# Kernel optimization log

Measured on AMD Instinct MI355X. Metric: run time of the kernel, lower is better.

## Reference

```python
import jax, jax.numpy as jnp
import numpy as np

N, E, C, NE, G, T = 20000, 320000, 32, 10, 64, 1000
NB, HID, LAYERS = 8, 64, 2
R_MAX, P_CUT, AVG_NEIGH = 5.0, 6, 16.0
LM = 16  # (max_ell+1)^2 spherical-harmonic components
L_OF_LM = jnp.array([0,1,1,1,2,2,2,2,2,3,3,3,3,3,3,3])


def sph_harm(u):
    # component-normalized real spherical harmonics up to l=3 on unit vectors u [E,3]
    x, y, z = u[:, 0], u[:, 1], u[:, 2]
    s3, s15, s5, s105, s7 = 3**0.5, 15**0.5, 5**0.5, 105**0.5, 7**0.5
    s35_8, s21_8 = (35.0/8.0)**0.5, (21.0/8.0)**0.5
    comps = [jnp.ones_like(x),
             s3*x, s3*y, s3*z,
             s15*x*y, s15*y*z, 0.5*s5*(3*z*z-1.0), s15*x*z, 0.5*s15*(x*x-y*y),
             s35_8*y*(3*x*x-y*y), s105*x*y*z, s21_8*y*(5*z*z-1.0),
             0.5*s7*(5*z*z*z-3*z), s21_8*x*(5*z*z-1.0),
             0.5*s105*z*(x*x-y*y), s35_8*x*(x*x-3*y*y)]
    return jnp.stack(comps, axis=-1)  # [E,16]


def radial_embed(r):
    # Bessel basis with polynomial cutoff (MACE RadialEmbeddingBlock)
    n = jnp.arange(1, NB + 1, dtype=r.dtype)
    rc = jnp.maximum(r, 1e-9)
    bessel = (2.0/R_MAX)**0.5 * jnp.sin(n[None, :]*jnp.pi*rc[:, None]/R_MAX) / rc[:, None]
    xr = r / R_MAX
    p = float(P_CUT)
    f = (1.0 - 0.5*(p+1)*(p+2)*xr**p + p*(p+2)*xr**(p+1) - 0.5*p*(p+1)*xr**(p+2))
    f = f * (xr < 1.0)
    return bessel * f[:, None]  # [E,NB]


def setup_inputs():
    key = jax.random.key(0)
    ks = jax.random.split(key, 16)
    positions = jax.random.normal(ks[0], (N, 3)) * 3.0
    species = jax.random.randint(ks[1], (N,), 0, NE)
    node_attrs = jax.nn.one_hot(species, NE, dtype=jnp.float32)
    edge_index = jax.random.randint(ks[2], (2, E), 0, N)
    shifts = jnp.zeros((E, 3), jnp.float32)
    batch = jnp.sort(jax.random.randint(ks[3], (N,), 0, G))
    t = jax.random.randint(ks[4], (G,), 0, T)
    eps = jax.random.normal(ks[5], (N, NE + 3))
    betas = jnp.linspace(1e-4, 0.02, T)
    alpha_bar = jnp.cumprod(1.0 - betas)
    sc = 0.1
    W_embed = sc * jax.random.normal(ks[6], (NE + 1, C))
    W_r1 = sc * jax.random.normal(ks[7], (LAYERS, NB, HID))
    W_r2 = sc * jax.random.normal(ks[8], (LAYERS, HID, C * 4))
    W_mix = sc * jax.random.normal(ks[9], (LAYERS, 4, C, C))
    W_sc = sc * jax.random.normal(ks[10], (NE, C))
    W_prod = sc * jax.random.normal(ks[11], (LAYERS, 3, C))
    W_ro_s = sc * jax.random.normal(ks[12], (LAYERS, C, NE))
    W_ro_v = sc * jax.random.normal(ks[13], (LAYERS, C))
    return {"positions": positions, "node_attrs": node_attrs, "shifts": shifts,
            "eps": eps, "alpha_bar": alpha_bar, "W_embed": W_embed, "W_r1": W_r1,
            "W_r2": W_r2, "W_mix": W_mix, "W_sc": W_sc, "W_prod": W_prod,
            "W_ro_s": W_ro_s, "W_ro_v": W_ro_v, "edge_index": edge_index,
            "batch": batch, "t": t}


def reference(positions, node_attrs, shifts, eps, alpha_bar, W_embed, W_r1, W_r2,
              W_mix, W_sc, W_prod, W_ro_s, W_ro_v, edge_index, batch, t):
    sender, receiver = edge_index[0], edge_index[1]
    # diffusion: noise positions and attrs (DDPM q(x_t|x_0))
    ab = alpha_bar[t][batch][:, None]                       # [N,1]
    attrs0 = node_attrs / 4.0
    pos_noisy = jnp.sqrt(ab) * positions + jnp.sqrt(1.0 - ab) * eps[:, -3:]
    attrs_noisy = jnp.sqrt(ab) * attrs0 + jnp.sqrt(1.0 - ab) * eps[:, :NE]
    tf = (t.astype(jnp.float32) / T)[batch][:, None]
    h = jnp.concatenate([attrs_noisy, tf], axis=-1) @ W_embed  # [N,C]
    # edge geometry
    vec = pos_noisy[receiver] - pos_noisy[sender] + shifts
    r = jnp.sqrt(jnp.sum(vec * vec, axis=-1) + 1e-12)
    Y = sph_harm(vec / r[:, None])                          # [E,16]
    ef = radial_embed(r)                                    # [E,NB]
    scalar = h
    pred = jnp.zeros((N, NE + 3), h.dtype)
    for layer in range(LAYERS):
        rw = jax.nn.silu(ef @ W_r1[layer]) @ W_r2[layer]    # [E,4C]
        rw = rw.reshape(E, C, 4)[:, :, L_OF_LM]             # [E,C,16]
        msg = rw * scalar[sender][:, :, None] * Y[:, None, :]
        agg = jax.ops.segment_sum(msg, receiver, num_segments=N) / AVG_NEIGH
        Wm = W_mix[layer][L_OF_LM]                          # [16,C,C]
        feats = jnp.einsum('nck,kcd->ndk', agg, Wm)         # per-l channel mix
        s = feats[:, :, 0]
        poly = W_prod[layer, 0] + W_prod[layer, 1] * s + W_prod[layer, 2] * s * s
        feats = feats * poly[:, :, None]                    # correlation-3 product
        if layer == 0:
            feats = feats.at[:, :, 0].add(attrs_noisy @ W_sc)  # element skip
        scalar = feats[:, :, 0]
        pred_s = scalar @ W_ro_s[layer]                     # [N,NE]
        pred_v = jnp.einsum('ncm,c->nm', feats[:, :, 1:4], W_ro_v[layer])  # [N,3]
        pred = pred + jnp.concatenate([pred_s, pred_v], axis=-1)
    err = (pred - eps) ** 2
    loss_pos = jax.ops.segment_sum(err[:, -3:].sum(-1), batch, num_segments=G)
    loss_lab = jax.ops.segment_sum(err[:, :NE].sum(-1), batch, num_segments=G)
    nn = jax.ops.segment_sum(jnp.ones((N,), pred.dtype), batch, num_segments=G)
    loss = 0.5 * (loss_pos + loss_lab) / (jnp.maximum(nn, 1.0) * (3 + NE))
    return loss
```

## Files before the change

### kernel.cpp

```cpp
#include <hip/hip_runtime.h>

typedef unsigned short ushort_t;
typedef unsigned int uint_t;

#define NN 20000
#define EE 320000
#define CC 32
#define NEL 10
#define GG 64
#define TTT 1000
#define NBB 8
#define HIDD 64
#define EPB 256
#define NTILE (EE / 16)

typedef __attribute__((ext_vector_type(8))) short bf16x8;
typedef __attribute__((ext_vector_type(4))) float f32x4;

__device__ __forceinline__ float bits2f(uint_t b) { union { uint_t u; float f; } v; v.u = b; return v.f; }
__device__ __forceinline__ ushort_t f2b(float f) {
  union { float f; uint_t u; } v; v.f = f;
  uint_t r = (v.u + 0x7fffu + ((v.u >> 16) & 1u)) >> 16;
  return (ushort_t)r;
}
__device__ __forceinline__ uint_t pk(float a, float b) {
  return (uint_t)f2b(a) | ((uint_t)f2b(b) << 16);
}
__device__ __forceinline__ float lo16(uint_t u) { return bits2f(u << 16); }
__device__ __forceinline__ float hi16(uint_t u) { return bits2f(u & 0xffff0000u); }

__global__ __launch_bounds__(256) void k_prep(
    const float* __restrict__ positions, const float* __restrict__ node_attrs,
    const float* __restrict__ eps, const float* __restrict__ alpha_bar,
    const float* __restrict__ W_embed, const float* __restrict__ W_sc,
    const int* __restrict__ batch, const int* __restrict__ tarr,
    float* __restrict__ pos_noisy, float* __restrict__ scalA,
    float* __restrict__ sc_skip, float* __restrict__ pred, int* __restrict__ deg)
{
  int n = blockIdx.x * 256 + threadIdx.x;
  if (n >= NN) return;
  deg[n] = 0;
  int g = batch[n];
  int tn = tarr[g];
  float ab = alpha_bar[tn];
  float sa = sqrtf(ab), sb = sqrtf(fmaxf(1.0f - ab, 0.0f));
#pragma unroll
  for (int j = 0; j < 3; ++j)
    pos_noisy[n * 3 + j] = sa * positions[n * 3 + j] + sb * eps[n * 13 + 10 + j];
  float an[10];
#pragma unroll
  for (int j = 0; j < 10; ++j)
    an[j] = sa * 0.25f * node_attrs[n * 10 + j] + sb * eps[n * 13 + j];
  float tf = (float)tn * (1.0f / (float)TTT);
  for (int d = 0; d < CC; ++d) {
    float h = tf * W_embed[10 * CC + d];
    float sk = 0.0f;
#pragma unroll
    for (int j = 0; j < 10; ++j) {
      h = fmaf(an[j], W_embed[j * CC + d], h);
      sk = fmaf(an[j], W_sc[j * CC + d], sk);
    }
    scalA[n * CC + d] = h;
    sc_skip[n * CC + d] = sk;
  }
#pragma unroll
  for (int j = 0; j < 13; ++j) pred[n * 13 + j] = 0.0f;
}

__global__ __launch_bounds__(256) void k_edge_deg(const int* __restrict__ ei,
    int* __restrict__ deg)
{
  int e = blockIdx.x * 256 + threadIdx.x;
  atomicAdd(&deg[ei[EE + e]], 1);
}

__global__ __launch_bounds__(1024) void k_scan(const int* __restrict__ deg,
    int* __restrict__ offs, int* __restrict__ cursor,
    float* __restrict__ lnum, float* __restrict__ lcnt)
{
  __shared__ int wsums[16];
  __shared__ int woffs[16];
  int tid = threadIdx.x, lane = tid & 63, wv = tid >> 6;
  if (tid < GG) { lnum[tid] = 0.0f; lcnt[tid] = 0.0f; }
  int base = tid * 20;
  int loc[20];
  int s = 0;
#pragma unroll
  for (int j = 0; j < 20; ++j) {
    int idx = base + j;
    int v = (idx < NN) ? deg[idx] : 0;
    loc[j] = s; s += v;
  }
  int inc = s;
  for (int o = 1; o < 64; o <<= 1) {
    int v = __shfl_up(inc, o, 64);
    if (lane >= o) inc += v;
  }
  if (lane == 63) wsums[wv] = inc;
  __syncthreads();
  if (wv == 0 && lane < 16) {
    int v = wsums[lane];
    int i2 = v;
    for (int o = 1; o < 16; o <<= 1) {
      int vv = __shfl_up(i2, o, 16);
      if (lane >= o) i2 += vv;
    }
    woffs[lane] = i2 - v;
  }
  __syncthreads();
  int texcl = woffs[wv] + (inc - s);
#pragma unroll
  for (int j = 0; j < 20; ++j) {
    int idx = base + j;
    if (idx < NN) { int v = texcl + loc[j]; offs[idx] = v; cursor[idx] = v; }
  }
  if (tid == 1023) offs[NN] = EE;
}

__global__ __launch_bounds__(256) void k_edge2(
    const float* __restrict__ pos_noisy, const float* __restrict__ shifts,
    const int* __restrict__ ei, int* __restrict__ cursor,
    ushort_t* __restrict__ Ys, ushort_t* __restrict__ efs, int* __restrict__ snds)
{
  int e = blockIdx.x * 256 + threadIdx.x;
  int snd = ei[e], rcv = ei[EE + e];
  float vx = pos_noisy[rcv * 3 + 0] - pos_noisy[snd * 3 + 0] + shifts[e * 3 + 0];
  float vy = pos_noisy[rcv * 3 + 1] - pos_noisy[snd * 3 + 1] + shifts[e * 3 + 1];
  float vz = pos_noisy[rcv * 3 + 2] - pos_noisy[snd * 3 + 2] + shifts[e * 3 + 2];
  float r2 = vx * vx + vy * vy + vz * vz + 1e-12f;
  float r = sqrtf(r2);
  float inv = 1.0f / r;
  float x = vx * inv, y = vy * inv, z = vz * inv;

  const float s3 = 1.7320508075688772f, s15 = 3.872983346207417f, s5 = 2.23606797749979f;
  const float s105 = 10.246950765959598f, s7 = 2.6457513110645907f;
  const float s35_8 = 2.091650066335189f, s21_8 = 1.6201851746019651f;
  float yv[16];
  yv[0] = 1.0f;
  yv[1] = s3 * x; yv[2] = s3 * y; yv[3] = s3 * z;
  yv[4] = s15 * x * y;
  yv[5] = s15 * y * z;
  yv[6] = 0.5f * s5 * (3.0f * z * z - 1.0f);
  yv[7] = s15 * x * z;
  yv[8] = 0.5f * s15 * (x * x - y * y);
  yv[9] = s35_8 * y * (3.0f * x * x - y * y);
  yv[10] = s105 * x * y * z;
  yv[11] = s21_8 * y * (5.0f * z * z - 1.0f);
  yv[12] = 0.5f * s7 * (5.0f * z * z * z - 3.0f * z);
  yv[13] = s21_8 * x * (5.0f * z * z - 1.0f);
  yv[14] = 0.5f * s105 * z * (x * x - y * y);
  yv[15] = s35_8 * x * (x * x - 3.0f * y * y);

  float rc = fmaxf(r, 1e-9f);
  float pref = 0.6324555320336759f / rc;
  float th = 0.6283185307179586f * rc;
  float s1 = __sinf(th), c1 = __cosf(th);
  float xr = r * 0.2f;
  float fcut = 0.0f;
  if (xr < 1.0f) {
    float x2 = xr * xr, x3 = x2 * xr;
    float x6 = x3 * x3, x7 = x6 * xr, x8 = x7 * xr;
    fcut = 1.0f - 28.0f * x6 + 48.0f * x7 - 21.0f * x8;
  }
  float efv[8];
  float sp = 0.0f, scur = s1, c2 = 2.0f * c1;
#pragma unroll
  for (int b = 0; b < 8; ++b) {
    efv[b] = pref * scur * fcut;
    float nx = c2 * scur - sp;
    sp = scur; scur = nx;
  }

  int slot = atomicAdd(&cursor[rcv], 1);
  snds[slot] = snd;
  uint4* Y4 = (uint4*)Ys;
  Y4[(size_t)slot * 2 + 0] = make_uint4(pk(yv[0], yv[1]), pk(yv[2], yv[3]),
                                        pk(yv[4], yv[5]), pk(yv[6], yv[7]));
  Y4[(size_t)slot * 2 + 1] = make_uint4(pk(yv[8], yv[9]), pk(yv[10], yv[11]),
                                        pk(yv[12], yv[13]), pk(yv[14], yv[15]));
  ((uint4*)efs)[slot] = make_uint4(pk(efv[0], efv[1]), pk(efv[2], efv[3]),
                                   pk(efv[4], efv[5]), pk(efv[6], efv[7]));
}

__global__ __launch_bounds__(256) void k_ytr(const ushort_t* __restrict__ Ys,
    ushort_t* __restrict__ YT)
{
  int idx = blockIdx.x * 256 + threadIdx.x;
  int tile = idx >> 4, k = idx & 15;
  ushort_t v[16];
#pragma unroll
  for (int el = 0; el < 16; ++el)
    v[el] = Ys[(size_t)(tile * 16 + el) * 16 + k];
  uint_t u[8];
#pragma unroll
  for (int p = 0; p < 8; ++p) u[p] = (uint_t)v[2 * p] | ((uint_t)v[2 * p + 1] << 16);
  uint4* o = (uint4*)(YT + (size_t)tile * 256 + (size_t)k * 16);
  o[0] = make_uint4(u[0], u[1], u[2], u[3]);
  o[1] = make_uint4(u[4], u[5], u[6], u[7]);
}

__global__ __launch_bounds__(256) void k_rw_mfma(
    const ushort_t* __restrict__ efs, const float* __restrict__ W_r1,
    const float* __restrict__ W_r2, const int* __restrict__ snds,
    const float* __restrict__ scal_in, ushort_t* __restrict__ rwT, int layer)
{
  __shared__ __align__(16) ushort_t w2t[128][72];
  __shared__ __align__(16) ushort_t h1[EPB][72];
  int tid = threadIdx.x;
  const float* W1g = W_r1 + layer * NBB * HIDD;
  const float* W2g = W_r2 + layer * HIDD * 128;
  for (int idx = tid; idx < HIDD * 128; idx += 256) {
    int k = idx >> 7, n = idx & 127;
    w2t[n][k] = f2b(W2g[idx]);
  }
  {
    int e = blockIdx.x * EPB + tid;
    uint4 q = ((const uint4*)efs)[e];
    float efr[8] = {lo16(q.x), hi16(q.x), lo16(q.y), hi16(q.y),
                    lo16(q.z), hi16(q.z), lo16(q.w), hi16(q.w)};
    for (int hc = 0; hc < 8; ++hc) {
      float v[8];
#pragma unroll
      for (int hh = 0; hh < 8; ++hh) {
        int h = hc * 8 + hh;
        float t = 0.0f;
#pragma unroll
        for (int b = 0; b < 8; ++b) t = fmaf(efr[b], W1g[b * HIDD + h], t);
        v[hh] = t / (1.0f + __expf(-t));
      }
      *(uint4*)&h1[tid][hc * 8] = make_uint4(pk(v[0], v[1]), pk(v[2], v[3]),
                                             pk(v[4], v[5]), pk(v[6], v[7]));
    }
  }
  __syncthreads();
  int w = tid >> 6, lane = tid & 63;
  int c = lane & 15, quad = lane >> 4;
  bf16x8 bfr[16];
#pragma unroll
  for (int nt = 0; nt < 8; ++nt)
#pragma unroll
    for (int kt = 0; kt < 2; ++kt)
      bfr[nt * 2 + kt] = *(const bf16x8*)&w2t[nt * 16 + c][kt * 32 + quad * 8];
  int mb0 = w * 64;
#pragma unroll
  for (int mt = 0; mt < 4; ++mt) {
    int mbase = mb0 + mt * 16;
    bf16x8 a0 = *(const bf16x8*)&h1[mbase + c][quad * 8];
    bf16x8 a1 = *(const bf16x8*)&h1[mbase + c][32 + quad * 8];
    size_t erow = (size_t)blockIdx.x * EPB + mbase + quad * 4;
    int4 sn = *(const int4*)&snds[erow];
    const float* sb0 = scal_in + (size_t)sn.x * CC;
    const float* sb1 = scal_in + (size_t)sn.y * CC;
    const float* sb2 = scal_in + (size_t)sn.z * CC;
    const float* sb3 = scal_in + (size_t)sn.w * CC;
    int tile = blockIdx.x * 16 + w * 4 + mt;
#pragma unroll
    for (int nt = 0; nt < 8; ++nt) {
      f32x4 acc = {0.0f, 0.0f, 0.0f, 0.0f};
      acc = __builtin_amdgcn_mfma_f32_16x16x32_bf16(a0, bfr[nt * 2 + 0], acc, 0, 0, 0);
      acc = __builtin_amdgcn_mfma_f32_16x16x32_bf16(a1, bfr[nt * 2 + 1], acc, 0, 0, 0);
      int col = nt * 16 + c;
      int cc = col >> 2;
      uint2 st;
      st.x = pk(acc[0] * sb0[cc], acc[1] * sb1[cc]);
      st.y = pk(acc[2] * sb2[cc], acc[3] * sb3[cc]);
      *(uint2*)(rwT + (size_t)tile * 2048 + (size_t)col * 16 + quad * 4) = st;
    }
  }
}

__global__ __launch_bounds__(256) void k_layer(
    const ushort_t* __restrict__ YT, const ushort_t* __restrict__ rwT,
    float* __restrict__ scal_out,
    const int* __restrict__ offs,
    const float* __restrict__ W_mix, const float* __restrict__ W_prod,
    const float* __restrict__ W_ro_s, const float* __restrict__ W_ro_v,
    const float* __restrict__ sc_skip, float* __restrict__ pred, int layer)
{
  __shared__ float lagg[4][CC][16];
  __shared__ float lf[4][CC][4];
  int w = threadIdx.x >> 6, lane = threadIdx.x & 63;
  int n = blockIdx.x * 4 + w;
  int c = lane & 15, quad = lane >> 4;
  int i0 = offs[n], i1 = offs[n + 1];
  int t0 = i0 >> 4, t1 = (i1 + 15) >> 4;
  int tsel = quad >> 1, half8 = quad & 1;
  f32x4 acc[8];
#pragma unroll
  for (int mt = 0; mt < 8; ++mt) acc[mt] = (f32x4){0.0f, 0.0f, 0.0f, 0.0f};

  for (int t = t0; t < t1; t += 2) {
    int ta = t + tsel;
    bf16x8 a[8];
    bf16x8 b;
    bool tv = (ta * 16 < i1) && (ta * 16 + 16 > i0);
    if (tv) {
      const bf16x8* ap = (const bf16x8*)rwT + (size_t)ta * 256 + c * 2 + half8;
#pragma unroll
      for (int mt = 0; mt < 8; ++mt) a[mt] = ap[mt * 32];
      b = ((const bf16x8*)YT)[(size_t)ta * 32 + c * 2 + half8];
      if (ta * 16 < i0 || ta * 16 + 16 > i1) {
        int sbase = ta * 16 + half8 * 8;
#pragma unroll
        for (int j = 0; j < 8; ++j) {
          int s = sbase + j;
          if (s < i0 || s >= i1) b[j] = 0;
        }
      }
    } else {
#pragma unroll
      for (int mt = 0; mt < 8; ++mt) a[mt] = (bf16x8){0, 0, 0, 0, 0, 0, 0, 0};
      b = (bf16x8){0, 0, 0, 0, 0, 0, 0, 0};
    }
#pragma unroll
    for (int mt = 0; mt < 8; ++mt)
      acc[mt] = __builtin_amdgcn_mfma_f32_16x16x32_bf16(a[mt], b, acc[mt], 0, 0, 0);
  }

  int lc = (c >= 1) + (c >= 4) + (c >= 9);
  const float inva = 1.0f / 16.0f;
#pragma unroll
  for (int mt = 0; mt < 8; ++mt) {
    float v = (lc == 0) ? acc[mt][0] : (lc == 1) ? acc[mt][1]
            : (lc == 2) ? acc[mt][2] : acc[mt][3];
    lagg[w][mt * 4 + quad][c] = v * inva;
  }
  __syncthreads();

  int c2 = lane >> 1;
  int kh = lane & 1;
  int kb = kh * 8;
  int d = c2;
  float ft[8] = {0, 0, 0, 0, 0, 0, 0, 0};
  const float* Wm = W_mix + layer * 4096;
  for (int cc2 = 0; cc2 < CC; ++cc2) {
    float m0 = Wm[cc2 * CC + d];
    float m1 = Wm[1024 + cc2 * CC + d];
    float m2 = Wm[2048 + cc2 * CC + d];
    float m3 = Wm[3072 + cc2 * CC + d];
    float u0 = kh ? m2 : m0;
    float u13 = kh ? m3 : m1;
    float u47 = kh ? m3 : m2;
    ft[0] = fmaf(lagg[w][cc2][kb + 0], u0, ft[0]);
    ft[1] = fmaf(lagg[w][cc2][kb + 1], u13, ft[1]);
    ft[2] = fmaf(lagg[w][cc2][kb + 2], u13, ft[2]);
    ft[3] = fmaf(lagg[w][cc2][kb + 3], u13, ft[3]);
    ft[4] = fmaf(lagg[w][cc2][kb + 4], u47, ft[4]);
    ft[5] = fmaf(lagg[w][cc2][kb + 5], u47, ft[5]);
    ft[6] = fmaf(lagg[w][cc2][kb + 6], u47, ft[6]);
    ft[7] = fmaf(lagg[w][cc2][kb + 7], u47, ft[7]);
  }
  float sv = __shfl(ft[0], lane & 62, 64);
  const float* Wp = W_prod + layer * 96;
  float p0 = Wp[d], p1 = Wp[32 + d], p2 = Wp[64 + d];
  float poly = fmaf(fmaf(p2, sv, p1), sv, p0);
#pragma unroll
  for (int j = 0; j < 8; ++j) ft[j] *= poly;
  if (layer == 0 && kh == 0) ft[0] += sc_skip[n * CC + d];
  if (kh == 0) {
    scal_out[n * CC + d] = ft[0];
    lf[w][d][0] = ft[0]; lf[w][d][1] = ft[1]; lf[w][d][2] = ft[2]; lf[w][d][3] = ft[3];
  }
  __syncthreads();
  if (lane < 13) {
    float sum = 0.0f;
    if (lane < 10) {
      const float* Wr = W_ro_s + layer * CC * NEL;
      for (int dd = 0; dd < CC; ++dd) sum = fmaf(lf[w][dd][0], Wr[dd * NEL + lane], sum);
    } else {
      int mm = lane - 10;
      const float* Wv = W_ro_v + layer * CC;
      for (int dd = 0; dd < CC; ++dd) sum = fmaf(lf[w][dd][1 + mm], Wv[dd], sum);
    }
    pred[n * 13 + lane] += sum;
  }
}

__global__ __launch_bounds__(256) void k_loss(const float* __restrict__ pred,
    const float* __restrict__ eps, const int* __restrict__ batch,
    float* __restrict__ lnum, float* __restrict__ lcnt)
{
  __shared__ float psum[GG];
  __shared__ int pcnt[GG];
  int tid = threadIdx.x;
  if (tid < GG) { psum[tid] = 0.0f; pcnt[tid] = 0; }
  __syncthreads();
  int n = blockIdx.x * 256 + tid;
  if (n < NN) {
    int g = batch[n];
    float sum = 0.0f;
#pragma unroll
    for (int j = 0; j < 13; ++j) {
      float dlt = pred[n * 13 + j] - eps[n * 13 + j];
      sum = fmaf(dlt, dlt, sum);
    }
    atomicAdd(&psum[g], sum);
    atomicAdd(&pcnt[g], 1);
  }
  __syncthreads();
  if (tid < GG && pcnt[tid] > 0) {
    atomicAdd(&lnum[tid], psum[tid]);
    atomicAdd(&lcnt[tid], (float)pcnt[tid]);
  }
}

__global__ void k_final(const float* __restrict__ lnum, const float* __restrict__ lcnt,
    float* __restrict__ out)
{
  int g = threadIdx.x;
  if (g < GG) {
    float nn = fmaxf(lcnt[g], 1.0f);
    out[g] = 0.5f * lnum[g] / (nn * 13.0f);
  }
}

extern "C" void kernel_launch(void* const* d_in, const int* in_sizes, int n_in,
                              void* d_out, int out_size, void* d_ws, size_t ws_size,
                              hipStream_t stream) {
  const float* positions  = (const float*)d_in[0];
  const float* node_attrs = (const float*)d_in[1];
  const float* shifts     = (const float*)d_in[2];
  const float* eps        = (const float*)d_in[3];
  const float* alpha_bar  = (const float*)d_in[4];
  const float* W_embed    = (const float*)d_in[5];
  const float* W_r1       = (const float*)d_in[6];
  const float* W_r2       = (const float*)d_in[7];
  const float* W_mix      = (const float*)d_in[8];
  const float* W_sc       = (const float*)d_in[9];
  const float* W_prod     = (const float*)d_in[10];
  const float* W_ro_s     = (const float*)d_in[11];
  const float* W_ro_v     = (const float*)d_in[12];
  const int* edge_index   = (const int*)d_in[13];
  const int* batch        = (const int*)d_in[14];
  const int* tarr         = (const int*)d_in[15];
  float* out = (float*)d_out;

  char* ws = (char*)d_ws;
  size_t off = 0;
  auto alloc = [&](size_t bytes) -> void* {
    void* p = ws + off;
    off = (off + bytes + 255) & ~(size_t)255;
    return p;
  };
  float* pos_noisy = (float*)alloc(NN * 3 * 4);
  float* scalA     = (float*)alloc(NN * CC * 4);
  float* scalB     = (float*)alloc(NN * CC * 4);
  float* sc_skip   = (float*)alloc(NN * CC * 4);
  float* pred      = (float*)alloc(NN * 13 * 4);
  ushort_t* Ys     = (ushort_t*)alloc((size_t)EE * 16 * 2);
  ushort_t* YT     = (ushort_t*)alloc((size_t)NTILE * 256 * 2);
  ushort_t* efs    = (ushort_t*)alloc((size_t)EE * 8 * 2);
  int* snds        = (int*)alloc((size_t)EE * 4);
  ushort_t* rwT    = (ushort_t*)alloc((size_t)NTILE * 2048 * 2);
  int* deg         = (int*)alloc(NN * 4);
  int* offs        = (int*)alloc((NN + 1) * 4);
  int* cursor      = (int*)alloc(NN * 4);
  float* lnum      = (float*)alloc(GG * 4);
  float* lcnt      = (float*)alloc(GG * 4);
  (void)ws_size; (void)in_sizes; (void)n_in; (void)out_size;

  const int NB_N = (NN + 255) / 256;
  const int NB_E = EE / 256;

  k_prep<<<NB_N, 256, 0, stream>>>(positions, node_attrs, eps, alpha_bar, W_embed,
                                   W_sc, batch, tarr, pos_noisy, scalA, sc_skip, pred, deg);
  k_edge_deg<<<NB_E, 256, 0, stream>>>(edge_index, deg);
  k_scan<<<1, 1024, 0, stream>>>(deg, offs, cursor, lnum, lcnt);
  k_edge2<<<NB_E, 256, 0, stream>>>(pos_noisy, shifts, edge_index, cursor, Ys, efs, snds);
  k_ytr<<<NB_E, 256, 0, stream>>>(Ys, YT);

  for (int layer = 0; layer < 2; ++layer) {
    const float* sin_p = (layer == 0) ? scalA : scalB;
    float* sout_p      = (layer == 0) ? scalB : scalA;
    k_rw_mfma<<<NB_E, 256, 0, stream>>>(efs, W_r1, W_r2, snds, sin_p, rwT, layer);
    k_layer<<<NN / 4, 256, 0, stream>>>(YT, rwT, sout_p, offs,
                                        W_mix, W_prod, W_ro_s, W_ro_v,
                                        sc_skip, pred, layer);
  }

  k_loss<<<NB_N, 256, 0, stream>>>(pred, eps, batch, lnum, lcnt);
  k_final<<<1, 64, 0, stream>>>(lnum, lcnt, out);
}
```

Before: 333.1 us.

## Fuse radial MLP into per-node aggregation using padded 16-edge CSR segments

Pads each node's CSR segment to a multiple of 16 edges, so every 16-edge tile belongs to exactly one receiver, and zero-fills the padding slots. The radial MLP and sender-scalar weighting now run inside the per-node aggregation kernel, so the large rwT intermediate is never written to or read back from global memory. W_r2 is pre-packed to bf16 once for both layers. The cost is extra padded work, up to roughly double the edge slots in the worst case, per-wave MFMAs that keep only half the K lanes busy, and load imbalance across nodes of different degree.

```diff
diff --git a/kernel.cpp b/kernel.cpp
--- a/kernel.cpp
+++ b/kernel.cpp
@@ -11,8 +11,7 @@
 #define TTT 1000
 #define NBB 8
 #define HIDD 64
-#define EPB 256
-#define NTILE (EE / 16)
+#define SLOTMAX 620032
 
 typedef __attribute__((ext_vector_type(8))) short bf16x8;
 typedef __attribute__((ext_vector_type(4))) float f32x4;
@@ -67,6 +66,15 @@
   for (int j = 0; j < 13; ++j) pred[n * 13 + j] = 0.0f;
 }
 
+__global__ __launch_bounds__(256) void k_wpack(const float* __restrict__ W_r2,
+    ushort_t* __restrict__ w2tg)
+{
+  int idx = blockIdx.x * 256 + threadIdx.x;
+  int l = idx >> 13, r = idx & 8191;
+  int n = r >> 6, k = r & 63;
+  w2tg[idx] = f2b(W_r2[l * 8192 + k * 128 + n]);
+}
+
 __global__ __launch_bounds__(256) void k_edge_deg(const int* __restrict__ ei,
     int* __restrict__ deg)
 {
@@ -88,7 +96,7 @@
 #pragma unroll
   for (int j = 0; j < 20; ++j) {
     int idx = base + j;
-    int v = (idx < NN) ? deg[idx] : 0;
+    int v = (idx < NN) ? ((deg[idx] + 15) & ~15) : 0;
     loc[j] = s; s += v;
   }
   int inc = s;
@@ -114,7 +122,25 @@
     int idx = base + j;
     if (idx < NN) { int v = texcl + loc[j]; offs[idx] = v; cursor[idx] = v; }
   }
-  if (tid == 1023) offs[NN] = EE;
+  if (tid == 1023) offs[NN] = texcl + s;
+}
+
+__global__ __launch_bounds__(256) void k_pad(const int* __restrict__ deg,
+    const int* __restrict__ offs, ushort_t* __restrict__ Ys,
+    ushort_t* __restrict__ efs, int* __restrict__ snds)
+{
+  int n = blockIdx.x * 256 + threadIdx.x;
+  if (n >= NN) return;
+  int d = deg[n];
+  int pd = (d + 15) & ~15;
+  int s0 = offs[n] + d, s1 = offs[n] + pd;
+  uint4 z = make_uint4(0, 0, 0, 0);
+  for (int s = s0; s < s1; ++s) {
+    ((uint4*)Ys)[(size_t)s * 2 + 0] = z;
+    ((uint4*)Ys)[(size_t)s * 2 + 1] = z;
+    ((uint4*)efs)[s] = z;
+    snds[s] = 0;
+  }
 }
 
 __global__ __launch_bounds__(256) void k_edge2(
@@ -183,10 +209,11 @@
 }
 
 __global__ __launch_bounds__(256) void k_ytr(const ushort_t* __restrict__ Ys,
-    ushort_t* __restrict__ YT)
+    ushort_t* __restrict__ YT, const int* __restrict__ offs)
 {
   int idx = blockIdx.x * 256 + threadIdx.x;
   int tile = idx >> 4, k = idx & 15;
+  if (tile * 16 >= offs[NN]) return;
   ushort_t v[16];
 #pragma unroll
   for (int el = 0; el < 16; ++el)
@@ -199,122 +226,96 @@
   o[1] = make_uint4(u[4], u[5], u[6], u[7]);
 }
 
-__global__ __launch_bounds__(256) void k_rw_mfma(
-    const ushort_t* __restrict__ efs, const float* __restrict__ W_r1,
-    const float* __restrict__ W_r2, const int* __restrict__ snds,
-    const float* __restrict__ scal_in, ushort_t* __restrict__ rwT, int layer)
-{
-  __shared__ __align__(16) ushort_t w2t[128][72];
-  __shared__ __align__(16) ushort_t h1[EPB][72];
-  int tid = threadIdx.x;
-  const float* W1g = W_r1 + layer * NBB * HIDD;
-  const float* W2g = W_r2 + layer * HIDD * 128;
-  for (int idx = tid; idx < HIDD * 128; idx += 256) {
-    int k = idx >> 7, n = idx & 127;
-    w2t[n][k] = f2b(W2g[idx]);
-  }
-  {
-    int e = blockIdx.x * EPB + tid;
-    uint4 q = ((const uint4*)efs)[e];
-    float efr[8] = {lo16(q.x), hi16(q.x), lo16(q.y), hi16(q.y),
-                    lo16(q.z), hi16(q.z), lo16(q.w), hi16(q.w)};
-    for (int hc = 0; hc < 8; ++hc) {
-      float v[8];
-#pragma unroll
-      for (int hh = 0; hh < 8; ++hh) {
-        int h = hc * 8 + hh;
-        float t = 0.0f;
-#pragma unroll
-        for (int b = 0; b < 8; ++b) t = fmaf(efr[b], W1g[b * HIDD + h], t);
-        v[hh] = t / (1.0f + __expf(-t));
-      }
-      *(uint4*)&h1[tid][hc * 8] = make_uint4(pk(v[0], v[1]), pk(v[2], v[3]),
-                                             pk(v[4], v[5]), pk(v[6], v[7]));
-    }
-  }
-  __syncthreads();
-  int w = tid >> 6, lane = tid & 63;
-  int c = lane & 15, quad = lane >> 4;
-  bf16x8 bfr[16];
-#pragma unroll
-  for (int nt = 0; nt < 8; ++nt)
-#pragma unroll
-    for (int kt = 0; kt < 2; ++kt)
-      bfr[nt * 2 + kt] = *(const bf16x8*)&w2t[nt * 16 + c][kt * 32 + quad * 8];
-  int mb0 = w * 64;
-#pragma unroll
-  for (int mt = 0; mt < 4; ++mt) {
-    int mbase = mb0 + mt * 16;
-    bf16x8 a0 = *(const bf16x8*)&h1[mbase + c][quad * 8];
-    bf16x8 a1 = *(const bf16x8*)&h1[mbase + c][32 + quad * 8];
-    size_t erow = (size_t)blockIdx.x * EPB + mbase + quad * 4;
-    int4 sn = *(const int4*)&snds[erow];
-    const float* sb0 = scal_in + (size_t)sn.x * CC;
-    const float* sb1 = scal_in + (size_t)sn.y * CC;
-    const float* sb2 = scal_in + (size_t)sn.z * CC;
-    const float* sb3 = scal_in + (size_t)sn.w * CC;
-    int tile = blockIdx.x * 16 + w * 4 + mt;
-#pragma unroll
-    for (int nt = 0; nt < 8; ++nt) {
-      f32x4 acc = {0.0f, 0.0f, 0.0f, 0.0f};
-      acc = __builtin_amdgcn_mfma_f32_16x16x32_bf16(a0, bfr[nt * 2 + 0], acc, 0, 0, 0);
-      acc = __builtin_amdgcn_mfma_f32_16x16x32_bf16(a1, bfr[nt * 2 + 1], acc, 0, 0, 0);
-      int col = nt * 16 + c;
-      int cc = col >> 2;
-      uint2 st;
-      st.x = pk(acc[0] * sb0[cc], acc[1] * sb1[cc]);
-      st.y = pk(acc[2] * sb2[cc], acc[3] * sb3[cc]);
-      *(uint2*)(rwT + (size_t)tile * 2048 + (size_t)col * 16 + quad * 4) = st;
-    }
-  }
-}
-
-__global__ __launch_bounds__(256) void k_layer(
-    const ushort_t* __restrict__ YT, const ushort_t* __restrict__ rwT,
-    float* __restrict__ scal_out,
-    const int* __restrict__ offs,
+__global__ __launch_bounds__(256, 3) void k_fused(
+    const ushort_t* __restrict__ efs, const ushort_t* __restrict__ YT,
+    const float* __restrict__ W_r1, const ushort_t* __restrict__ w2tg,
+    const int* __restrict__ snds, const float* __restrict__ scal_in,
+    float* __restrict__ scal_out, const int* __restrict__ offs,
     const float* __restrict__ W_mix, const float* __restrict__ W_prod,
     const float* __restrict__ W_ro_s, const float* __restrict__ W_ro_v,
     const float* __restrict__ sc_skip, float* __restrict__ pred, int layer)
 {
+  __shared__ float w1s[NBB * HIDD];
+  __shared__ __align__(16) ushort_t h1s[4][16][72];
+  __shared__ __align__(16) ushort_t rws[4][128][24];
   __shared__ float lagg[4][CC][16];
   __shared__ float lf[4][CC][4];
-  int w = threadIdx.x >> 6, lane = threadIdx.x & 63;
+  int tid = threadIdx.x;
+  const float* W1g = W_r1 + layer * NBB * HIDD;
+  for (int i = tid; i < NBB * HIDD; i += 256) w1s[i] = W1g[i];
+  __syncthreads();
+
+  int w = tid >> 6, lane = tid & 63;
   int n = blockIdx.x * 4 + w;
   int c = lane & 15, quad = lane >> 4;
   int i0 = offs[n], i1 = offs[n + 1];
-  int t0 = i0 >> 4, t1 = (i1 + 15) >> 4;
-  int tsel = quad >> 1, half8 = quad & 1;
+  const ushort_t* w2l = w2tg + layer * (HIDD * 128);
+  int eh = lane >> 2, sub = lane & 3;
+
   f32x4 acc[8];
 #pragma unroll
   for (int mt = 0; mt < 8; ++mt) acc[mt] = (f32x4){0.0f, 0.0f, 0.0f, 0.0f};
 
-  for (int t = t0; t < t1; t += 2) {
-    int ta = t + tsel;
-    bf16x8 a[8];
-    bf16x8 b;
-    bool tv = (ta * 16 < i1) && (ta * 16 + 16 > i0);
-    if (tv) {
-      const bf16x8* ap = (const bf16x8*)rwT + (size_t)ta * 256 + c * 2 + half8;
-#pragma unroll
-      for (int mt = 0; mt < 8; ++mt) a[mt] = ap[mt * 32];
-      b = ((const bf16x8*)YT)[(size_t)ta * 32 + c * 2 + half8];
-      if (ta * 16 < i0 || ta * 16 + 16 > i1) {
-        int sbase = ta * 16 + half8 * 8;
-#pragma unroll
-        for (int j = 0; j < 8; ++j) {
-          int s = sbase + j;
-          if (s < i0 || s >= i1) b[j] = 0;
+  const bf16x8 bz = (bf16x8){0, 0, 0, 0, 0, 0, 0, 0};
+
+  for (int sb = i0; sb < i1; sb += 16) {
+    {
+      uint4 q = ((const uint4*)efs)[sb + eh];
+      float efr[8] = {lo16(q.x), hi16(q.x), lo16(q.y), hi16(q.y),
+                      lo16(q.z), hi16(q.z), lo16(q.w), hi16(q.w)};
+#pragma unroll
+      for (int g = 0; g < 2; ++g) {
+        float v[8];
+#pragma unroll
+        for (int hh = 0; hh < 8; ++hh) {
+          int h = sub * 16 + g * 8 + hh;
+          float t = 0.0f;
+#pragma unroll
+          for (int b = 0; b < 8; ++b) t = fmaf(efr[b], w1s[b * HIDD + h], t);
+          v[hh] = t / (1.0f + __expf(-t));
         }
+        *(uint4*)&h1s[w][eh][sub * 16 + g * 8] =
+            make_uint4(pk(v[0], v[1]), pk(v[2], v[3]), pk(v[4], v[5]), pk(v[6], v[7]));
       }
-    } else {
-#pragma unroll
-      for (int mt = 0; mt < 8; ++mt) a[mt] = (bf16x8){0, 0, 0, 0, 0, 0, 0, 0};
-      b = (bf16x8){0, 0, 0, 0, 0, 0, 0, 0};
-    }
-#pragma unroll
-    for (int mt = 0; mt < 8; ++mt)
-      acc[mt] = __builtin_amdgcn_mfma_f32_16x16x32_bf16(a[mt], b, acc[mt], 0, 0, 0);
+    }
+    __builtin_amdgcn_wave_barrier();
+    {
+      bf16x8 a0 = *(const bf16x8*)&h1s[w][c][quad * 8];
+      bf16x8 a1 = *(const bf16x8*)&h1s[w][c][32 + quad * 8];
+      int4 sn = *(const int4*)&snds[sb + quad * 4];
+      const float* s0 = scal_in + (size_t)sn.x * CC;
+      const float* s1 = scal_in + (size_t)sn.y * CC;
+      const float* s2 = scal_in + (size_t)sn.z * CC;
+      const float* s3 = scal_in + (size_t)sn.w * CC;
+#pragma unroll
+      for (int nt = 0; nt < 8; ++nt) {
+        bf16x8 b0 = *(const bf16x8*)&w2l[(nt * 16 + c) * 64 + quad * 8];
+        bf16x8 b1 = *(const bf16x8*)&w2l[(nt * 16 + c) * 64 + 32 + quad * 8];
+        f32x4 r = {0.0f, 0.0f, 0.0f, 0.0f};
+        r = __builtin_amdgcn_mfma_f32_16x16x32_bf16(a0, b0, r, 0, 0, 0);
+        r = __builtin_amdgcn_mfma_f32_16x16x32_bf16(a1, b1, r, 0, 0, 0);
+        int col = nt * 16 + c, ch = col >> 2;
+        uint2 st;
+        st.x = pk(r[0] * s0[ch], r[1] * s1[ch]);
+        st.y = pk(r[2] * s2[ch], r[3] * s3[ch]);
+        *(uint2*)&rws[w][col][quad * 4] = st;
+      }
+    }
+    __builtin_amdgcn_wave_barrier();
+    {
+      int ptile = sb >> 4;
+      bf16x8 b = bz;
+      if (quad < 2)
+        b = *(const bf16x8*)&YT[(size_t)ptile * 256 + c * 16 + quad * 8];
+#pragma unroll
+      for (int mt = 0; mt < 8; ++mt) {
+        bf16x8 a = bz;
+        if (quad < 2)
+          a = *(const bf16x8*)&rws[w][mt * 16 + c][quad * 8];
+        acc[mt] = __builtin_amdgcn_mfma_f32_16x16x32_bf16(a, b, acc[mt], 0, 0, 0);
+      }
+    }
+    __builtin_amdgcn_wave_barrier();
   }
 
   int lc = (c >= 1) + (c >= 4) + (c >= 9);
@@ -447,11 +448,11 @@
   float* scalB     = (float*)alloc(NN * CC * 4);
   float* sc_skip   = (float*)alloc(NN * CC * 4);
   float* pred      = (float*)alloc(NN * 13 * 4);
-  ushort_t* Ys     = (ushort_t*)alloc((size_t)EE * 16 * 2);
-  ushort_t* YT     = (ushort_t*)alloc((size_t)NTILE * 256 * 2);
-  ushort_t* efs    = (ushort_t*)alloc((size_t)EE * 8 * 2);
-  int* snds        = (int*)alloc((size_t)EE * 4);
-  ushort_t* rwT    = (ushort_t*)alloc((size_t)NTILE * 2048 * 2);
+  ushort_t* Ys     = (ushort_t*)alloc((size_t)SLOTMAX * 16 * 2);
+  ushort_t* YT     = (ushort_t*)alloc((size_t)SLOTMAX * 16 * 2);
+  ushort_t* efs    = (ushort_t*)alloc((size_t)SLOTMAX * 8 * 2);
+  int* snds        = (int*)alloc((size_t)SLOTMAX * 4);
+  ushort_t* w2tg   = (ushort_t*)alloc(2 * HIDD * 128 * 2);
   int* deg         = (int*)alloc(NN * 4);
   int* offs        = (int*)alloc((NN + 1) * 4);
   int* cursor      = (int*)alloc(NN * 4);
@@ -461,20 +462,22 @@
 
   const int NB_N = (NN + 255) / 256;
   const int NB_E = EE / 256;
+  const int NB_T = SLOTMAX / 256;
 
   k_prep<<<NB_N, 256, 0, stream>>>(positions, node_attrs, eps, alpha_bar, W_embed,
                                    W_sc, batch, tarr, pos_noisy, scalA, sc_skip, pred, deg);
+  k_wpack<<<64, 256, 0, stream>>>(W_r2, w2tg);
   k_edge_deg<<<NB_E, 256, 0, stream>>>(edge_index, deg);
   k_scan<<<1, 1024, 0, stream>>>(deg, offs, cursor, lnum, lcnt);
+  k_pad<<<NB_N, 256, 0, stream>>>(deg, offs, Ys, efs, snds);
   k_edge2<<<NB_E, 256, 0, stream>>>(pos_noisy, shifts, edge_index, cursor, Ys, efs, snds);
-  k_ytr<<<NB_E, 256, 0, stream>>>(Ys, YT);
+  k_ytr<<<NB_T, 256, 0, stream>>>(Ys, YT, offs);
 
   for (int layer = 0; layer < 2; ++layer) {
     const float* sin_p = (layer == 0) ? scalA : scalB;
     float* sout_p      = (layer == 0) ? scalB : scalA;
-    k_rw_mfma<<<NB_E, 256, 0, stream>>>(efs, W_r1, W_r2, snds, sin_p, rwT, layer);
-    k_layer<<<NN / 4, 256, 0, stream>>>(YT, rwT, sout_p, offs,
-                                        W_mix, W_prod, W_ro_s, W_ro_v,
+    k_fused<<<NN / 4, 256, 0, stream>>>(efs, YT, W_r1, w2tg, snds, sin_p, sout_p,
+                                        offs, W_mix, W_prod, W_ro_s, W_ro_v,
                                         sc_skip, pred, layer);
   }
 
```

Result: slower. 428.7 us (+28.7%).

## Prepack bf16 weights once, use MFMA for channel mixing, relax block barriers

Applied to the files above, without the earlier changes.

A new kernel converts W_r2 (transposed) and W_mix to bf16 once per call. k_rw_mfma then reads its B fragments directly from global memory instead of building a per-block LDS copy. k_layer replaces the scalar per-l channel-mix loop with a bf16 MFMA over a padded shared buffer. Block __syncthreads are swapped for wave barriers because each wave only touches its own LDS slice. The mix now runs in bf16 instead of fp32, which costs precision.

```diff
diff --git a/kernel.cpp b/kernel.cpp
--- a/kernel.cpp
+++ b/kernel.cpp
@@ -65,6 +65,24 @@
   }
 #pragma unroll
   for (int j = 0; j < 13; ++j) pred[n * 13 + j] = 0.0f;
+}
+
+__global__ __launch_bounds__(256) void k_wpack(const float* __restrict__ W_r2,
+    const float* __restrict__ W_mix, ushort_t* __restrict__ w2tg,
+    ushort_t* __restrict__ wmixb)
+{
+  int idx = blockIdx.x * 256 + threadIdx.x;
+  if (idx < 16384) {
+    int l = idx >> 13, r = idx & 8191;
+    int n = r >> 6, k = r & 63;
+    w2tg[idx] = f2b(W_r2[l * 8192 + k * 128 + n]);
+  } else {
+    int r = idx - 16384;
+    int l = r >> 12, r2 = r & 4095;
+    int col = r2 >> 5, ch = r2 & 31;
+    int lq = col >> 5, d = col & 31;
+    wmixb[r] = f2b(W_mix[l * 4096 + lq * 1024 + ch * 32 + d]);
+  }
 }
 
 __global__ __launch_bounds__(256) void k_edge_deg(const int* __restrict__ ei,
@@ -201,18 +219,13 @@
 
 __global__ __launch_bounds__(256) void k_rw_mfma(
     const ushort_t* __restrict__ efs, const float* __restrict__ W_r1,
-    const float* __restrict__ W_r2, const int* __restrict__ snds,
+    const ushort_t* __restrict__ w2tg, const int* __restrict__ snds,
     const float* __restrict__ scal_in, ushort_t* __restrict__ rwT, int layer)
 {
-  __shared__ __align__(16) ushort_t w2t[128][72];
   __shared__ __align__(16) ushort_t h1[EPB][72];
   int tid = threadIdx.x;
   const float* W1g = W_r1 + layer * NBB * HIDD;
-  const float* W2g = W_r2 + layer * HIDD * 128;
-  for (int idx = tid; idx < HIDD * 128; idx += 256) {
-    int k = idx >> 7, n = idx & 127;
-    w2t[n][k] = f2b(W2g[idx]);
-  }
+  const ushort_t* w2l = w2tg + layer * (HIDD * 128);
   {
     int e = blockIdx.x * EPB + tid;
     uint4 q = ((const uint4*)efs)[e];
@@ -232,7 +245,7 @@
                                              pk(v[4], v[5]), pk(v[6], v[7]));
     }
   }
-  __syncthreads();
+  __builtin_amdgcn_wave_barrier();
   int w = tid >> 6, lane = tid & 63;
   int c = lane & 15, quad = lane >> 4;
   bf16x8 bfr[16];
@@ -240,7 +253,7 @@
   for (int nt = 0; nt < 8; ++nt)
 #pragma unroll
     for (int kt = 0; kt < 2; ++kt)
-      bfr[nt * 2 + kt] = *(const bf16x8*)&w2t[nt * 16 + c][kt * 32 + quad * 8];
+      bfr[nt * 2 + kt] = *(const bf16x8*)&w2l[(nt * 16 + c) * 64 + kt * 32 + quad * 8];
   int mb0 = w * 64;
 #pragma unroll
   for (int mt = 0; mt < 4; ++mt) {
@@ -273,11 +286,12 @@
     const ushort_t* __restrict__ YT, const ushort_t* __restrict__ rwT,
     float* __restrict__ scal_out,
     const int* __restrict__ offs,
-    const float* __restrict__ W_mix, const float* __restrict__ W_prod,
+    const ushort_t* __restrict__ wmixb, const float* __restrict__ W_prod,
     const float* __restrict__ W_ro_s, const float* __restrict__ W_ro_v,
     const float* __restrict__ sc_skip, float* __restrict__ pred, int layer)
 {
-  __shared__ float lagg[4][CC][16];
+  __shared__ float lagg[4][CC][17];
+  __shared__ float lfeat[4][CC][17];
   __shared__ float lf[4][CC][4];
   int w = threadIdx.x >> 6, lane = threadIdx.x & 63;
   int n = blockIdx.x * 4 + w;
@@ -325,32 +339,43 @@
             : (lc == 2) ? acc[mt][2] : acc[mt][3];
     lagg[w][mt * 4 + quad][c] = v * inva;
   }
-  __syncthreads();
-
-  int c2 = lane >> 1;
+  __builtin_amdgcn_wave_barrier();
+
+  float av[8];
+#pragma unroll
+  for (int j = 0; j < 8; ++j) av[j] = lagg[w][quad * 8 + j][c];
+  union { uint_t u[4]; bf16x8 b; } cv;
+  cv.u[0] = pk(av[0], av[1]); cv.u[1] = pk(av[2], av[3]);
+  cv.u[2] = pk(av[4], av[5]); cv.u[3] = pk(av[6], av[7]);
+  bf16x8 afrag = cv.b;
+  const ushort_t* wmixl = wmixb + layer * 4096;
+  f32x4 o[8];
+#pragma unroll
+  for (int nt = 0; nt < 8; ++nt) {
+    bf16x8 bfm = *(const bf16x8*)&wmixl[(nt * 16 + c) * 32 + quad * 8];
+    f32x4 z = {0.0f, 0.0f, 0.0f, 0.0f};
+    o[nt] = __builtin_amdgcn_mfma_f32_16x16x32_bf16(afrag, bfm, z, 0, 0, 0);
+  }
+#pragma unroll
+  for (int jj = 0; jj < 4; ++jj) {
+    int k = quad * 4 + jj;
+    int lq = (k >= 1) + (k >= 4) + (k >= 9);
+    float vlo = (lq == 0) ? o[0][jj] : (lq == 1) ? o[2][jj]
+              : (lq == 2) ? o[4][jj] : o[6][jj];
+    float vhi = (lq == 0) ? o[1][jj] : (lq == 1) ? o[3][jj]
+              : (lq == 2) ? o[5][jj] : o[7][jj];
+    lfeat[w][c][k] = vlo;
+    lfeat[w][c + 16][k] = vhi;
+  }
+  __builtin_amdgcn_wave_barrier();
+
+  int d = lane >> 1;
   int kh = lane & 1;
   int kb = kh * 8;
-  int d = c2;
-  float ft[8] = {0, 0, 0, 0, 0, 0, 0, 0};
-  const float* Wm = W_mix + layer * 4096;
-  for (int cc2 = 0; cc2 < CC; ++cc2) {
-    float m0 = Wm[cc2 * CC + d];
-    float m1 = Wm[1024 + cc2 * CC + d];
-    float m2 = Wm[2048 + cc2 * CC + d];
-    float m3 = Wm[3072 + cc2 * CC + d];
-    float u0 = kh ? m2 : m0;
-    float u13 = kh ? m3 : m1;
-    float u47 = kh ? m3 : m2;
-    ft[0] = fmaf(lagg[w][cc2][kb + 0], u0, ft[0]);
-    ft[1] = fmaf(lagg[w][cc2][kb + 1], u13, ft[1]);
-    ft[2] = fmaf(lagg[w][cc2][kb + 2], u13, ft[2]);
-    ft[3] = fmaf(lagg[w][cc2][kb + 3], u13, ft[3]);
-    ft[4] = fmaf(lagg[w][cc2][kb + 4], u47, ft[4]);
-    ft[5] = fmaf(lagg[w][cc2][kb + 5], u47, ft[5]);
-    ft[6] = fmaf(lagg[w][cc2][kb + 6], u47, ft[6]);
-    ft[7] = fmaf(lagg[w][cc2][kb + 7], u47, ft[7]);
-  }
-  float sv = __shfl(ft[0], lane & 62, 64);
+  float ft[8];
+#pragma unroll
+  for (int j = 0; j < 8; ++j) ft[j] = lfeat[w][d][kb + j];
+  float sv = lfeat[w][d][0];
   const float* Wp = W_prod + layer * 96;
   float p0 = Wp[d], p1 = Wp[32 + d], p2 = Wp[64 + d];
   float poly = fmaf(fmaf(p2, sv, p1), sv, p0);
@@ -361,7 +386,7 @@
     scal_out[n * CC + d] = ft[0];
     lf[w][d][0] = ft[0]; lf[w][d][1] = ft[1]; lf[w][d][2] = ft[2]; lf[w][d][3] = ft[3];
   }
-  __syncthreads();
+  __builtin_amdgcn_wave_barrier();
   if (lane < 13) {
     float sum = 0.0f;
     if (lane < 10) {
@@ -448,10 +473,12 @@
   float* sc_skip   = (float*)alloc(NN * CC * 4);
   float* pred      = (float*)alloc(NN * 13 * 4);
   ushort_t* Ys     = (ushort_t*)alloc((size_t)EE * 16 * 2);
-  ushort_t* YT     = (ushort_t*)alloc((size_t)NTILE * 256 * 2);
+  ushort_t* YT     = (ushort_t*)alloc((size_t)EE * 16 * 2);
   ushort_t* efs    = (ushort_t*)alloc((size_t)EE * 8 * 2);
   int* snds        = (int*)alloc((size_t)EE * 4);
-  ushort_t* rwT    = (ushort_t*)alloc((size_t)NTILE * 2048 * 2);
+  ushort_t* rwT    = (ushort_t*)alloc((size_t)EE * 128 * 2);
+  ushort_t* w2tg   = (ushort_t*)alloc(2 * HIDD * 128 * 2);
+  ushort_t* wmixb  = (ushort_t*)alloc(2 * 128 * CC * 2);
   int* deg         = (int*)alloc(NN * 4);
   int* offs        = (int*)alloc((NN + 1) * 4);
   int* cursor      = (int*)alloc(NN * 4);
@@ -464,6 +491,7 @@
 
   k_prep<<<NB_N, 256, 0, stream>>>(positions, node_attrs, eps, alpha_bar, W_embed,
                                    W_sc, batch, tarr, pos_noisy, scalA, sc_skip, pred, deg);
+  k_wpack<<<96, 256, 0, stream>>>(W_r2, W_mix, w2tg, wmixb);
   k_edge_deg<<<NB_E, 256, 0, stream>>>(edge_index, deg);
   k_scan<<<1, 1024, 0, stream>>>(deg, offs, cursor, lnum, lcnt);
   k_edge2<<<NB_E, 256, 0, stream>>>(pos_noisy, shifts, edge_index, cursor, Ys, efs, snds);
@@ -472,9 +500,9 @@
   for (int layer = 0; layer < 2; ++layer) {
     const float* sin_p = (layer == 0) ? scalA : scalB;
     float* sout_p      = (layer == 0) ? scalB : scalA;
-    k_rw_mfma<<<NB_E, 256, 0, stream>>>(efs, W_r1, W_r2, snds, sin_p, rwT, layer);
+    k_rw_mfma<<<NB_E, 256, 0, stream>>>(efs, W_r1, w2tg, snds, sin_p, rwT, layer);
     k_layer<<<NN / 4, 256, 0, stream>>>(YT, rwT, sout_p, offs,
-                                        W_mix, W_prod, W_ro_s, W_ro_v,
+                                        wmixb, W_prod, W_ro_s, W_ro_v,
                                         sc_skip, pred, layer);
   }
 
```

New measurement: 315.4 us. 1.06x faster.
